# Kernel tuning notes

Measured on AMD Instinct MI355X. Metric: run time of the kernel, lower is better.

## Reference

```python
import jax, jax.numpy as jnp
import numpy as np

INNER_LR = 0.01  # args['update_lr']
T, N, D, H = 100, 100, 1024, 8192


def setup_inputs() -> dict:
    key = jax.random.key(0)
    ks = jax.random.split(key, 6)
    return {
        "x_traj": jax.random.normal(ks[0], (T, D), jnp.float32),
        "y_traj": jax.random.normal(ks[1], (T, 1), jnp.float32),
        "x_rand": jax.random.normal(ks[2], (N, D), jnp.float32),
        "y_rand": jax.random.normal(ks[3], (N, 1), jnp.float32),
        # learned meta parameters of the columnar net
        "W": jax.random.normal(ks[4], (D, H), jnp.float32) * (1.0 / np.sqrt(D)),
        "b": jnp.zeros((H,), jnp.float32),
        # adaptation parameter (last-layer prediction weights)
        "w0": jax.random.normal(ks[5], (H,), jnp.float32) * 0.01,
    }


def reference(x_traj, y_traj, x_rand, y_rand, W, b, w0):
    lr = jnp.float32(INNER_LR)

    def net(x):
        h = jnp.tanh(x @ W + b)          # [H] hidden / rnn_state
        return h

    # ---- trajectory loop: update TH, online update of w, update TW ----
    def traj_step(carry, inp):
        w, TW_W, TW_b = carry
        x, tgt = inp
        h = net(x)
        y = jnp.dot(w, h)                # scalar prediction
        dact = 1.0 - h * h
        # update_TH: TH <- per-column grads of hidden wrt meta params
        TH_W = x[:, None] * dact[None, :]   # [D,H]
        TH_b = dact                          # [H]
        err = tgt - y
        # online_update (adaptation param), happens BEFORE update_TW
        w_new = w + lr * err * h
        # update_TW (uses post-update prediction params, old_state = h)
        TW_W = TW_W + lr * err * TH_W - lr * h[None, :] * (w_new[None, :] * TH_W + h[None, :] * TW_W)
        TW_b = TW_b + lr * err * TH_b - lr * h * (w_new * TH_b + h * TW_b)
        return (w_new, TW_W, TW_b), None

    init = (w0, jnp.zeros_like(W), jnp.zeros_like(b))
    (w_f, TW_W, TW_b), _ = jax.lax.scan(traj_step, init, (x_traj, y_traj[:, 0]))

    # ---- random (meta-loss) loop: accumulate meta-gradients ----
    def rand_step(carry, inp):
        gW, gb, loss = carry
        x, tgt = inp
        h = net(x)
        y = jnp.dot(w_f, h)
        dact = 1.0 - h * h
        TH_W = x[:, None] * dact[None, :]
        TH_b = dact
        err = tgt - y
        loss = loss + (y - tgt) ** 2     # F.mse_loss on scalars
        gW = gW + (-err) * (w_f[None, :] * TH_W + TW_W * h[None, :])
        gb = gb + (-err) * (w_f * TH_b + TW_b * h)
        return (gW, gb, loss), None

    init2 = (jnp.zeros_like(W), jnp.zeros_like(b), jnp.float32(0.0))
    (gW, gb, total_loss), _ = jax.lax.scan(rand_step, init2, (x_rand, y_rand[:, 0]))

    return (total_loss / N, gW, gb)
```

## Files before the change

### kernel.cpp

```cpp
#include <hip/hip_runtime.h>
#include <hip/hip_bf16.h>
#include <math.h>

#define TT 100
#define NN 100
#define DD 1024
#define HH 8192
#define ILR 0.01f

typedef short bf16x8 __attribute__((ext_vector_type(8)));
typedef float f32x4 __attribute__((ext_vector_type(4)));


__device__ __forceinline__ float wave_sum64(float v) {
#pragma unroll
  for (int off = 32; off; off >>= 1) v += __shfl_xor(v, off, 64);
  return v;
}

__device__ __forceinline__ unsigned short f2bf(float x) {
  __hip_bfloat16 b = __float2bfloat16(x);
  return *(unsigned short*)&b;
}
__device__ __forceinline__ float bf2f(unsigned short u) {
  __hip_bfloat16 b = *(__hip_bfloat16*)&u;
  return __bfloat162float(b);
}

__global__ __launch_bounds__(256) void k0_frag(const float* __restrict__ xt,
                                               const float* __restrict__ xr,
                                               unsigned short* __restrict__ XA2f,
                                               unsigned short* __restrict__ XT2f) {
  const int tx = threadIdx.x & 31;
  const int ty = threadIdx.x >> 5;
  const int m0 = blockIdx.x * 32;
  const int r0 = blockIdx.y * 32;
#pragma unroll
  for (int i = 0; i < 4; i++) {
    const int r = r0 + ty + i * 8;
    const int m = m0 + tx;
    float v = 0.f;
    if (r < 200) {
      const float* src = (r < TT) ? (xt + r * DD) : (xr + (r - TT) * DD);
      v = src[m];
    }
    const unsigned short h = f2bf(v);
    const unsigned short l = f2bf(v - bf2f(h));
    {
      const int idx = ((((r >> 4) * 32 + (m >> 5)) * 64) +
                       ((m >> 3) & 3) * 16 + (r & 15)) * 8 + (m & 7);
      XA2f[idx] = h;
      XA2f[idx + 262144] = l;
    }
    {
      const int idx = ((((m >> 4) * 8 + (r >> 5)) * 64) +
                       ((r >> 3) & 3) * 16 + (m & 15)) * 8 + (r & 7);
      XT2f[idx] = h;
      XT2f[idx + 262144] = l;
    }
  }
}

__global__ __launch_bounds__(256, 4) void k1_mfma7(const unsigned short* __restrict__ XA2f,
                                                   const float* __restrict__ W,
                                                   const float* __restrict__ bias,
                                                   float* __restrict__ Hall) {
  __shared__ unsigned short Bsm[2 * 4096];
  const int tid = threadIdx.x;
  const int wid = tid >> 6;
  const int lane = tid & 63;
  const int flat = blockIdx.x;
  const int m8 = flat & 7;
  const int r_tile = (flat >> 3) & 3;
  const int chi = flat >> 5;
  const int c_tile = chi * 8 + m8;
  const int row0 = r_tile * 64;
  const int col0 = c_tile * 32;
  const int wr = wid >> 1;
  const int wc = wid & 1;

  const int sc = tid & 31;
  const int ko = tid >> 5;
  const int sbase = (((sc >> 4) * 2 + (ko >> 2)) * 64 + (ko & 3) * 16 + (sc & 15)) * 8;

  f32x4 acc[2];
#pragma unroll
  for (int i = 0; i < 2; i++) {
    f32x4 zv = {0.f, 0.f, 0.f, 0.f};
    acc[i] = zv;
  }

  float wv[8];
#define K1_LOADW(CH)                                                           \
  _Pragma("unroll") for (int e = 0; e < 8; e++) wv[e] =                        \
      W[(size_t)((CH) * 64 + ko * 8 + e) * HH + col0 + sc];
#define K1_CVT(BUF)                                                            \
  {                                                                            \
    bf16x8 Hv, Lv;                                                             \
    _Pragma("unroll") for (int e = 0; e < 8; e++) {                            \
      const unsigned short hh = f2bf(wv[e]);                                   \
      Hv[e] = (short)hh;                                                       \
      Lv[e] = (short)f2bf(wv[e] - bf2f(hh));                                   \
    }                                                                          \
    unsigned short* d = Bsm + (BUF) * 4096 + sbase;                            \
    *(bf16x8*)d = Hv;                                                          \
    *(bf16x8*)(d + 2048) = Lv;                                                 \
  }
#define K1_MFMA(CHL, BUF)                                                      \
  _Pragma("unroll") for (int kb = 0; kb < 2; kb++) {                           \
    const int kbg = (CHL) * 2 + kb;                                            \
    bf16x8 ah[2], al[2], bh, bl;                                               \
    _Pragma("unroll") for (int mf = 0; mf < 2; mf++) {                         \
      const int tA = r_tile * 4 + wr * 2 + mf;                                 \
      const unsigned short* pa =                                               \
          XA2f + (size_t)((tA * 32 + kbg) * 64 + lane) * 8;                    \
      ah[mf] = *(const bf16x8*)pa;                                             \
      al[mf] = *(const bf16x8*)(pa + 262144);                                  \
    }                                                                          \
    {                                                                          \
      const unsigned short* pb =                                               \
          Bsm + (BUF) * 4096 + ((wc * 2 + kb) * 64 + lane) * 8;                \
      bh = *(const bf16x8*)pb;                                                 \
      bl = *(const bf16x8*)(pb + 2048);                                        \
    }                                                                          \
    _Pragma("unroll") for (int mf = 0; mf < 2; mf++) {                         \
      acc[mf] = __builtin_amdgcn_mfma_f32_16x16x32_bf16(ah[mf], bh, acc[mf], 0, 0, 0); \
      acc[mf] = __builtin_amdgcn_mfma_f32_16x16x32_bf16(ah[mf], bl, acc[mf], 0, 0, 0); \
      acc[mf] = __builtin_amdgcn_mfma_f32_16x16x32_bf16(al[mf], bh, acc[mf], 0, 0, 0); \
    }                                                                          \
  }

  K1_LOADW(0)
  K1_CVT(0)
  __syncthreads();

#pragma unroll 1
  for (int ch = 0; ch < 16; ch++) {
    if (ch < 15) { K1_LOADW(ch + 1) }
    K1_MFMA(ch, ch & 1)
    if (ch < 15) {
      K1_CVT((ch + 1) & 1)
      __syncthreads();
    }
  }
#undef K1_LOADW
#undef K1_CVT
#undef K1_MFMA

  const int l15 = lane & 15;
  const int drow = (lane >> 4) * 4;
#pragma unroll
  for (int mf = 0; mf < 2; mf++) {
    const int gr = row0 + wr * 32 + mf * 16 + drow;
    const int gc = col0 + wc * 16 + l15;
    const float bv = bias[gc];
#pragma unroll
    for (int r = 0; r < 4; r++) {
      const int row = gr + r;
      if (row < 200)
        Hall[(size_t)row * HH + gc] = tanhf(acc[mf][r] + bv);
    }
  }
}

__global__ __launch_bounds__(64) void k2a_gram(const float* __restrict__ Ht,
                                               const float* __restrict__ w0,
                                               float* __restrict__ Gp,
                                               float* __restrict__ y0p) {
  __shared__ float red[64 * 65];
  const int task = blockIdx.x;
  const int z = blockIdx.y;
  const int lane = threadIdx.x;
  const int kb = z * 512;
  if (task < 91) {
    int a = 0, rem = task;
    while (rem >= 13 - a) { rem -= 13 - a; a++; }
    const int b = a + rem;
    const float* Ra = Ht + (size_t)(a * 8) * HH + kb;
    const float* Rb = Ht + (size_t)(b * 8) * HH + kb;
    float acc[8][8];
#pragma unroll
    for (int r = 0; r < 8; r++)
#pragma unroll
      for (int c = 0; c < 8; c++) acc[r][c] = 0.f;
#pragma unroll
    for (int i = 0; i < 2; i++) {
      const int k = (lane + i * 64) * 4;
      float4 x[8];
#pragma unroll
      for (int r = 0; r < 8; r++) x[r] = *(const float4*)(Ra + (size_t)r * HH + k);
#pragma unroll
      for (int c = 0; c < 8; c++) {
        const float4 u = *(const float4*)(Rb + (size_t)c * HH + k);
#pragma unroll
        for (int r = 0; r < 8; r++) {
          acc[r][c] = fmaf(x[r].x, u.x, acc[r][c]);
          acc[r][c] = fmaf(x[r].y, u.y, acc[r][c]);
          acc[r][c] = fmaf(x[r].z, u.z, acc[r][c]);
          acc[r][c] = fmaf(x[r].w, u.w, acc[r][c]);
        }
      }
    }
#pragma unroll
    for (int r = 0; r < 8; r++)
#pragma unroll
      for (int c = 0; c < 8; c++) red[lane * 65 + r * 8 + c] = acc[r][c];
    __syncthreads();
    float s = 0.f;
#pragma unroll
    for (int i = 0; i < 64; i++) s += red[i * 65 + lane];
    Gp[(size_t)task * 1024 + z * 64 + lane] = s;
  } else {
    const int a = task - 91;
    const float* R = Ht + (size_t)(a * 8) * HH + kb;
    float acc[8] = {0.f, 0.f, 0.f, 0.f, 0.f, 0.f, 0.f, 0.f};
#pragma unroll
    for (int i = 0; i < 2; i++) {
      const int k = (lane + i * 64) * 4;
      const float4 wvv = *(const float4*)(w0 + kb + k);
#pragma unroll
      for (int r = 0; r < 8; r++) {
        const float4 x = *(const float4*)(R + (size_t)r * HH + k);
        acc[r] += x.x * wvv.x + x.y * wvv.y + x.z * wvv.z + x.w * wvv.w;
      }
    }
#pragma unroll
    for (int r = 0; r < 8; r++) acc[r] = wave_sum64(acc[r]);
    if (lane == 0) {
#pragma unroll
      for (int r = 0; r < 8; r++) y0p[a * 128 + z * 8 + r] = acc[r];
    }
  }
}

__global__ __launch_bounds__(128) void k2b_reduce(const float* __restrict__ Gp,
                                                  const float* __restrict__ y0p,
                                                  float* __restrict__ G,
                                                  float* __restrict__ y0) {
  const int blk = blockIdx.x;
  const int t = threadIdx.x;
  if (blk < 91) {
    if (t < 64) {
      float s = 0.f;
#pragma unroll
      for (int z = 0; z < 16; z++) s += Gp[(size_t)blk * 1024 + z * 64 + t];
      int a = 0, rem = blk;
      while (rem >= 13 - a) { rem -= 13 - a; a++; }
      const int b = a + rem;
      const int gr = a * 8 + (t >> 3);
      const int gc = b * 8 + (t & 7);
      if (gr < 100 && gc < 100) {
        G[gr * 100 + gc] = s;
        G[gc * 100 + gr] = s;
      }
    }
  } else {
    if (t < 104) {
      float s = 0.f;
#pragma unroll
      for (int z = 0; z < 16; z++) s += y0p[(t >> 3) * 128 + z * 8 + (t & 7)];
      if (t < 100) y0[t] = s;
    }
  }
}

__global__ __launch_bounds__(256) void k3_solve2(const float* __restrict__ G,
                                                 const float* __restrict__ y0,
                                                 const float* __restrict__ ytraj,
                                                 float* __restrict__ errT) {
  __shared__ float Gs[100 * 100];
  __shared__ float rhs[100];
  const int tid = threadIdx.x;
  for (int idx = tid; idx < 10000; idx += 256) Gs[idx] = G[idx];
  if (tid < 100) rhs[tid] = ytraj[tid] - y0[tid];
  __syncthreads();
  if (tid >= 64) return;
  const int l = tid;
  float acc_lo = 0.f, acc_hi = 0.f;
  float err_lo = 0.f, err_hi = 0.f;
#pragma unroll 4
  for (int t = 0; t < TT; t++) {
    const float a = (t < 64) ? __shfl(acc_lo, t) : __shfl(acc_hi, t - 64);
    const float err = rhs[t] - ILR * a;
    if (t < 64) {
      if (l == t) err_lo = err;
    } else {
      if (l == t - 64) err_hi = err;
    }
    const float g_lo = Gs[t * 100 + l];
    if (l > t) acc_lo = fmaf(err, g_lo, acc_lo);
    if (l < 36) {
      const float g_hi = Gs[t * 100 + 64 + l];
      if (64 + l > t) acc_hi = fmaf(err, g_hi, acc_hi);
    }
  }
  errT[l] = err_lo;
  if (l < 36) errT[64 + l] = err_hi;
}

__global__ __launch_bounds__(64) void k4a_scan(const float* __restrict__ Ht,
                                               const float* __restrict__ errT,
                                               float* __restrict__ Sp,
                                               float* __restrict__ Pp) {
  __shared__ float es[20];
  const int c = blockIdx.y;
  const int t0 = c * 20;
  if (threadIdx.x < 20) es[threadIdx.x] = errT[t0 + threadIdx.x];
  __syncthreads();
  const int j = blockIdx.x * 64 + threadIdx.x;
  float h[20];
#pragma unroll
  for (int u = 0; u < 20; u++) h[u] = Ht[(size_t)(t0 + u) * HH + j];
  float S = 0.f, P = 1.f;
#pragma unroll
  for (int u = 0; u < 20; u++) S += es[u] * h[u];
#pragma unroll
  for (int u = 0; u < 20; u++) P *= (1.f - ILR * h[u] * h[u]);
  Sp[(size_t)c * HH + j] = S;
  Pp[(size_t)c * HH + j] = P;
}

__global__ __launch_bounds__(64) void k4b_emit(const float* __restrict__ Ht,
                                               const float* __restrict__ errT,
                                               const float* __restrict__ w0,
                                               const float* __restrict__ Sp,
                                               const float* __restrict__ Pp,
                                               float* __restrict__ Ct,
                                               float* __restrict__ wf) {
  __shared__ float es[20];
  const int c = blockIdx.y;
  const int t0 = c * 20;
  if (threadIdx.x < 20) es[threadIdx.x] = errT[t0 + threadIdx.x];
  __syncthreads();
  const int j = blockIdx.x * 64 + threadIdx.x;
  float Sv[5], Pv[5];
#pragma unroll
  for (int q = 0; q < 5; q++) {
    Sv[q] = Sp[(size_t)q * HH + j];
    Pv[q] = Pp[(size_t)q * HH + j];
  }
  float w = w0[j];
#pragma unroll
  for (int q = 0; q < 5; q++)
    if (q < c) w += ILR * Sv[q];
  float PA = 1.f;
#pragma unroll
  for (int q = 0; q < 5; q++)
    if (q > c) PA *= Pv[q];
  float h[20];
#pragma unroll
  for (int u = 0; u < 20; u++) h[u] = Ht[(size_t)(t0 + u) * HH + j];
  float ct[20];
#pragma unroll
  for (int u = 0; u < 20; u++) {
    const float e = es[u];
    w += ILR * e * h[u];
    ct[u] = ILR * (1.f - h[u] * h[u]) * (e - h[u] * w);
  }
  float r = PA;
#pragma unroll
  for (int u = 19; u >= 0; u--) {
    Ct[(size_t)(t0 + u) * HH + j] = ct[u] * r;
    r *= (1.f - ILR * h[u] * h[u]);
  }
  if (c == 4) wf[j] = w;
}

__global__ __launch_bounds__(256) void k5_pred(const float* __restrict__ Hr,
                                               const float* __restrict__ wf,
                                               const float* __restrict__ yr,
                                               float* __restrict__ e_r) {
  const int i = blockIdx.x;
  const int tid = threadIdx.x;
  const float* row = Hr + (size_t)i * HH;
  float p = 0.f;
#pragma unroll
  for (int c = tid * 4; c < HH; c += 1024) {
    const float4 h4 = *(const float4*)(row + c);
    const float4 w4 = *(const float4*)(wf + c);
    p += h4.x * w4.x + h4.y * w4.y + h4.z * w4.z + h4.w * w4.w;
  }
  p = wave_sum64(p);
  __shared__ float ps[4];
  if ((tid & 63) == 0) ps[tid >> 6] = p;
  __syncthreads();
  if (tid == 0) {
    const float y = ps[0] + ps[1] + ps[2] + ps[3];
    e_r[i] = y - yr[i];
  }
}

__global__ __launch_bounds__(64) void k6a_v(const float* __restrict__ Hr,
                                            const float* __restrict__ e_r,
                                            float* __restrict__ Vp,
                                            float* __restrict__ loss_out) {
  __shared__ float es[20];
  const int c = blockIdx.y;
  const int i0 = c * 20;
  if (threadIdx.x < 20) es[threadIdx.x] = e_r[i0 + threadIdx.x];
  __syncthreads();
  if (blockIdx.x == 0 && c == 0) {
    const int l = threadIdx.x;
    float s = e_r[l] * e_r[l];
    if (l < 36) {
      const float q = e_r[l + 64];
      s += q * q;
    }
    s = wave_sum64(s);
    if (l == 0) loss_out[0] = s / (float)NN;
  }
  const int j = blockIdx.x * 64 + threadIdx.x;
  float h[20];
#pragma unroll
  for (int u = 0; u < 20; u++) h[u] = Hr[(size_t)(i0 + u) * HH + j];
  float S = 0.f;
#pragma unroll
  for (int u = 0; u < 20; u++) S += es[u] * h[u];
  Vp[(size_t)c * HH + j] = S;
}

__global__ __launch_bounds__(256) void k6b_m(const float* __restrict__ Hr,
                                             const float* __restrict__ e_r,
                                             const float* __restrict__ wf,
                                             const float* __restrict__ Ct,
                                             const float* __restrict__ Vp,
                                             unsigned short* __restrict__ MT2f,
                                             float* __restrict__ gbp) {
  __shared__ float es[100];
  const int tid = threadIdx.x;
  for (int i = tid; i < 100; i += 256) es[i] = e_r[i];
  __syncthreads();
  const int j = blockIdx.x * 256 + tid;
  const int iMo = blockIdx.y;
  float v = 0.f;
#pragma unroll
  for (int c = 0; c < 5; c++) v += Vp[(size_t)c * HH + j];
  const float wfj = wf[j];
  float m[8];
#pragma unroll
  for (int e = 0; e < 8; e++) {
    const int iM = iMo * 8 + e;
    if (iM < 100) {
      m[e] = v * Ct[(size_t)iM * HH + j];
    } else if (iM < 200) {
      const float h = Hr[(size_t)(iM - 100) * HH + j];
      m[e] = es[iM - 100] * wfj * (1.f - h * h);
    } else {
      m[e] = 0.f;
    }
  }
  bf16x8 Hv, Lv;
  float gbs = 0.f;
#pragma unroll
  for (int e = 0; e < 8; e++) {
    const unsigned short hh = f2bf(m[e]);
    Hv[e] = (short)hh;
    Lv[e] = (short)f2bf(m[e] - bf2f(hh));
    gbs += m[e];
  }
  const int idx = (((j >> 4) * 8 + (iMo >> 2)) * 64 + (iMo & 3) * 16 + (j & 15)) * 8;
  *(bf16x8*)&MT2f[idx] = Hv;
  *(bf16x8*)&MT2f[idx + 2097152] = Lv;
  if (iMo < 25) gbp[(size_t)iMo * HH + j] = gbs;
}

__global__ __launch_bounds__(256) void k7_mfma3(const unsigned short* __restrict__ XT2f,
                                                const unsigned short* __restrict__ MT2f,
                                                const float* __restrict__ gbp,
                                                float* __restrict__ gW,
                                                float* __restrict__ gb_out) {
  const int tid = threadIdx.x;
  if (blockIdx.x == 0 && tid < 128) {
    const int j = blockIdx.y * 128 + tid;
    float g = 0.f;
#pragma unroll
    for (int q = 0; q < 25; q++) g += gbp[(size_t)q * HH + j];
    gb_out[j] = g;
  }
  const int l = tid & 63;
  const int wid = tid >> 6;
  const int m0 = blockIdx.x * 128 + (wid >> 1) * 64;
  const int n0 = blockIdx.y * 128 + (wid & 1) * 64;
  const int tA0 = m0 >> 4;
  const int tN0 = n0 >> 4;

  f32x4 acc[4][4];
#pragma unroll
  for (int i = 0; i < 4; i++)
#pragma unroll
    for (int j = 0; j < 4; j++) {
      f32x4 z = {0.f, 0.f, 0.f, 0.f};
      acc[i][j] = z;
    }

#pragma unroll 2
  for (int kb = 0; kb < 8; kb++) {
    bf16x8 ah[4], al[4], bh[4], bl[4];
#pragma unroll
    for (int i = 0; i < 4; i++) {
      const unsigned short* pa = XT2f + (size_t)(((tA0 + i) * 8 + kb) * 64 + l) * 8;
      ah[i] = *(const bf16x8*)pa;
      al[i] = *(const bf16x8*)(pa + 262144);
      const unsigned short* pb = MT2f + (size_t)(((tN0 + i) * 8 + kb) * 64 + l) * 8;
      bh[i] = *(const bf16x8*)pb;
      bl[i] = *(const bf16x8*)(pb + 2097152);
    }
#pragma unroll
    for (int i = 0; i < 4; i++)
#pragma unroll
      for (int j = 0; j < 4; j++) {
        acc[i][j] = __builtin_amdgcn_mfma_f32_16x16x32_bf16(ah[i], bh[j], acc[i][j], 0, 0, 0);
        acc[i][j] = __builtin_amdgcn_mfma_f32_16x16x32_bf16(ah[i], bl[j], acc[i][j], 0, 0, 0);
        acc[i][j] = __builtin_amdgcn_mfma_f32_16x16x32_bf16(al[i], bh[j], acc[i][j], 0, 0, 0);
      }
  }
  const int l15 = l & 15;
  const int drow = (l >> 4) * 4;
#pragma unroll
  for (int i = 0; i < 4; i++)
#pragma unroll
    for (int j = 0; j < 4; j++) {
      float* dst = gW + (size_t)(m0 + i * 16 + drow) * HH + n0 + j * 16 + l15;
#pragma unroll
      for (int r = 0; r < 4; r++) dst[(size_t)r * HH] = acc[i][j][r];
    }
}

extern "C" void kernel_launch(void* const* d_in, const int* in_sizes, int n_in,
                              void* d_out, int out_size, void* d_ws, size_t ws_size,
                              hipStream_t stream) {
  (void)in_sizes; (void)n_in; (void)out_size; (void)ws_size;
  const float* xt = (const float*)d_in[0];
  const float* yt = (const float*)d_in[1];
  const float* xr = (const float*)d_in[2];
  const float* yr = (const float*)d_in[3];
  const float* W = (const float*)d_in[4];
  const float* bias = (const float*)d_in[5];
  const float* w0 = (const float*)d_in[6];
  float* out = (float*)d_out;
  float* ws = (float*)d_ws;

  float* Hall = ws;
  float* Ht = Hall;
  float* Hr = Hall + TT * HH;
  unsigned short* XA2f = (unsigned short*)(Hall + 200 * HH);
  unsigned short* XT2f = XA2f + 524288;
  float* scratch = (float*)(XT2f + 524288);
  float* Ct = scratch;
  unsigned short* MT2f = (unsigned short*)(scratch + 819200);
  float* Gp = scratch + 819200 + 2097152;
  float* y0p = Gp + 91 * 1024;
  float* Sp = y0p + 13 * 128;
  float* Pp = Sp + 5 * HH;
  float* Vp = Pp + 5 * HH;
  float* gbp = Vp + 5 * HH;
  float* G = gbp + 25 * HH;
  float* y0v = G + TT * TT;
  float* errT = y0v + TT;
  float* e_r = errT + TT;
  float* wf = e_r + NN;

  k0_frag<<<dim3(32, 8), 256, 0, stream>>>(xt, xr, XA2f, XT2f);
  k1_mfma7<<<1024, 256, 0, stream>>>(XA2f, W, bias, Hall);
  k2a_gram<<<dim3(104, 16), 64, 0, stream>>>(Ht, w0, Gp, y0p);
  k2b_reduce<<<92, 128, 0, stream>>>(Gp, y0p, G, y0v);
  k3_solve2<<<1, 256, 0, stream>>>(G, y0v, yt, errT);
  k4a_scan<<<dim3(128, 5), 64, 0, stream>>>(Ht, errT, Sp, Pp);
  k4b_emit<<<dim3(128, 5), 64, 0, stream>>>(Ht, errT, w0, Sp, Pp, Ct, wf);
  k5_pred<<<NN, 256, 0, stream>>>(Hr, wf, yr, e_r);
  k6a_v<<<dim3(128, 5), 64, 0, stream>>>(Hr, e_r, Vp, out);
  k6b_m<<<dim3(32, 32), 256, 0, stream>>>(Hr, e_r, wf, Ct, Vp, MT2f, gbp);
  k7_mfma3<<<dim3(8, 64), 256, 0, stream>>>(XT2f, MT2f, gbp, out + 1,
                                            out + 1 + (size_t)DD * HH);
}
```

Baseline: 105.7 us.

## Deepen W prefetch in k1 to two chunks and fold Gram reduction into solver

The GEMM kernel now keeps two register sets for W chunks, so loads run two chunks ahead of the MFMA work and global-load latency is better hidden. This raises register pressure. Separately, the k2b reduce kernel is merged into the single-block solve kernel, which sums the Gram and y0 partials straight into shared memory. That removes one launch and a global round trip, but the reduction now runs on only one block.

```diff
diff --git a/kernel.cpp b/kernel.cpp
--- a/kernel.cpp
+++ b/kernel.cpp
@@ -61,7 +61,7 @@
   }
 }
 
-__global__ __launch_bounds__(256, 4) void k1_mfma7(const unsigned short* __restrict__ XA2f,
+__global__ __launch_bounds__(256, 4) void k1_mfma8(const unsigned short* __restrict__ XA2f,
                                                    const float* __restrict__ W,
                                                    const float* __restrict__ bias,
                                                    float* __restrict__ Hall) {
@@ -90,17 +90,17 @@
     acc[i] = zv;
   }
 
-  float wv[8];
-#define K1_LOADW(CH)                                                           \
-  _Pragma("unroll") for (int e = 0; e < 8; e++) wv[e] =                        \
+  float wvA[8], wvB[8];
+#define K1_LOADW(CH, REGS)                                                     \
+  _Pragma("unroll") for (int e = 0; e < 8; e++) REGS[e] =                      \
       W[(size_t)((CH) * 64 + ko * 8 + e) * HH + col0 + sc];
-#define K1_CVT(BUF)                                                            \
+#define K1_CVT(REGS, BUF)                                                      \
   {                                                                            \
     bf16x8 Hv, Lv;                                                             \
     _Pragma("unroll") for (int e = 0; e < 8; e++) {                            \
-      const unsigned short hh = f2bf(wv[e]);                                   \
+      const unsigned short hh = f2bf(REGS[e]);                                 \
       Hv[e] = (short)hh;                                                       \
-      Lv[e] = (short)f2bf(wv[e] - bf2f(hh));                                   \
+      Lv[e] = (short)f2bf(REGS[e] - bf2f(hh));                                 \
     }                                                                          \
     unsigned short* d = Bsm + (BUF) * 4096 + sbase;                            \
     *(bf16x8*)d = Hv;                                                          \
@@ -130,16 +130,21 @@
     }                                                                          \
   }
 
-  K1_LOADW(0)
-  K1_CVT(0)
+  K1_LOADW(0, wvA)
+  K1_LOADW(1, wvB)
+  K1_CVT(wvA, 0)
   __syncthreads();
 
 #pragma unroll 1
-  for (int ch = 0; ch < 16; ch++) {
-    if (ch < 15) { K1_LOADW(ch + 1) }
-    K1_MFMA(ch, ch & 1)
-    if (ch < 15) {
-      K1_CVT((ch + 1) & 1)
+  for (int ch2 = 0; ch2 < 16; ch2 += 2) {
+    if (ch2 + 2 < 16) { K1_LOADW(ch2 + 2, wvA) }
+    K1_MFMA(ch2, 0)
+    K1_CVT(wvB, 1)
+    __syncthreads();
+    if (ch2 + 3 < 16) { K1_LOADW(ch2 + 3, wvB) }
+    K1_MFMA(ch2 + 1, 1)
+    if (ch2 + 2 < 16) {
+      K1_CVT(wvA, 0)
       __syncthreads();
     }
   }
@@ -233,46 +238,35 @@
   }
 }
 
-__global__ __launch_bounds__(128) void k2b_reduce(const float* __restrict__ Gp,
-                                                  const float* __restrict__ y0p,
-                                                  float* __restrict__ G,
-                                                  float* __restrict__ y0) {
-  const int blk = blockIdx.x;
-  const int t = threadIdx.x;
-  if (blk < 91) {
-    if (t < 64) {
-      float s = 0.f;
-#pragma unroll
-      for (int z = 0; z < 16; z++) s += Gp[(size_t)blk * 1024 + z * 64 + t];
-      int a = 0, rem = blk;
-      while (rem >= 13 - a) { rem -= 13 - a; a++; }
-      const int b = a + rem;
-      const int gr = a * 8 + (t >> 3);
-      const int gc = b * 8 + (t & 7);
-      if (gr < 100 && gc < 100) {
-        G[gr * 100 + gc] = s;
-        G[gc * 100 + gr] = s;
-      }
-    }
-  } else {
-    if (t < 104) {
-      float s = 0.f;
-#pragma unroll
-      for (int z = 0; z < 16; z++) s += y0p[(t >> 3) * 128 + z * 8 + (t & 7)];
-      if (t < 100) y0[t] = s;
-    }
-  }
-}
-
-__global__ __launch_bounds__(256) void k3_solve2(const float* __restrict__ G,
-                                                 const float* __restrict__ y0,
+__global__ __launch_bounds__(256) void k3_merged(const float* __restrict__ Gp,
+                                                 const float* __restrict__ y0p,
                                                  const float* __restrict__ ytraj,
                                                  float* __restrict__ errT) {
   __shared__ float Gs[100 * 100];
   __shared__ float rhs[100];
   const int tid = threadIdx.x;
-  for (int idx = tid; idx < 10000; idx += 256) Gs[idx] = G[idx];
-  if (tid < 100) rhs[tid] = ytraj[tid] - y0[tid];
+  for (int idx = tid; idx < 91 * 64; idx += 256) {
+    const int task = idx >> 6;
+    const int t = idx & 63;
+    float s = 0.f;
+#pragma unroll
+    for (int z = 0; z < 16; z++) s += Gp[(size_t)task * 1024 + z * 64 + t];
+    int a = 0, rem = task;
+    while (rem >= 13 - a) { rem -= 13 - a; a++; }
+    const int b = a + rem;
+    const int gr = a * 8 + (t >> 3);
+    const int gc = b * 8 + (t & 7);
+    if (gr < 100 && gc < 100) {
+      Gs[gr * 100 + gc] = s;
+      Gs[gc * 100 + gr] = s;
+    }
+  }
+  if (tid < 100) {
+    float s = 0.f;
+#pragma unroll
+    for (int z = 0; z < 16; z++) s += y0p[(tid >> 3) * 128 + z * 8 + (tid & 7)];
+    rhs[tid] = ytraj[tid] - s;
+  }
   __syncthreads();
   if (tid >= 64) return;
   const int l = tid;
@@ -554,17 +548,14 @@
   float* Pp = Sp + 5 * HH;
   float* Vp = Pp + 5 * HH;
   float* gbp = Vp + 5 * HH;
-  float* G = gbp + 25 * HH;
-  float* y0v = G + TT * TT;
-  float* errT = y0v + TT;
+  float* errT = gbp + 25 * HH;
   float* e_r = errT + TT;
   float* wf = e_r + NN;
 
   k0_frag<<<dim3(32, 8), 256, 0, stream>>>(xt, xr, XA2f, XT2f);
-  k1_mfma7<<<1024, 256, 0, stream>>>(XA2f, W, bias, Hall);
+  k1_mfma8<<<1024, 256, 0, stream>>>(XA2f, W, bias, Hall);
   k2a_gram<<<dim3(104, 16), 64, 0, stream>>>(Ht, w0, Gp, y0p);
-  k2b_reduce<<<92, 128, 0, stream>>>(Gp, y0p, G, y0v);
-  k3_solve2<<<1, 256, 0, stream>>>(G, y0v, yt, errT);
+  k3_merged<<<1, 256, 0, stream>>>(Gp, y0p, yt, errT);
   k4a_scan<<<dim3(128, 5), 64, 0, stream>>>(Ht, errT, Sp, Pp);
   k4b_emit<<<dim3(128, 5), 64, 0, stream>>>(Ht, errT, w0, Sp, Pp, Ct, wf);
   k5_pred<<<NN, 256, 0, stream>>>(Hr, wf, yr, e_r);
```

Measured after the change: 111.7 us. 5.7% more time.
